# Kernel optimization log

Hardware: AMD Instinct MI355X
Metric: run time of the kernel (lower is better)

Reference implementation:

```python
import jax, jax.numpy as jnp
import numpy as np

V, E, B, K = 100000, 128, 65536, 10


def setup_inputs() -> dict:
    key = jax.random.key(0)
    k1, k2, k3, k4 = jax.random.split(key, 4)
    center_words = jax.random.randint(k1, (B,), 0, V, dtype=jnp.int64 if jax.config.jax_enable_x64 else jnp.int32)
    outside_words = jax.random.randint(k2, (B,), 0, V, dtype=center_words.dtype)
    # torch.multinomial over uniform noise_dist == uniform sampling of negatives
    neg_input_ids = jax.random.randint(k3, (B, K), 0, V, dtype=center_words.dtype)
    # word_embeddings.weight.data.uniform_(-1, 1)
    emb = jax.random.uniform(k4, (V, E), dtype=jnp.float32, minval=-1.0, maxval=1.0)
    return {"center_words": center_words, "outside_words": outside_words,
            "neg_input_ids": neg_input_ids, "emb": emb}


def reference(center_words, outside_words, neg_input_ids, emb):
    em_center = emb[center_words]            # [B, E]
    em_outside = emb[outside_words]          # [B, E]
    pos_dot = jnp.sum(em_center * em_outside, axis=1)          # [B]
    true_pair_loss = -jax.nn.log_sigmoid(pos_dot)              # [B]
    em_neg = emb[neg_input_ids]                                # [B, K, E]
    neg_dot = -jnp.einsum('bke,be->bk', em_neg, em_center)     # [B, K]
    noise_pair_loss = -jnp.sum(jax.nn.log_sigmoid(neg_dot), axis=1)  # [B]
    return jnp.mean(true_pair_loss + noise_pair_loss)
```

## Files before the change

### kernel.cpp

```cpp
#include <hip/hip_runtime.h>
#include <math.h>
#include <stdint.h>

#define BB 65536
#define KK 10
#define EE 128
#define VV 100000

constexpr int BLOCK = 256;
constexpr int BPB   = 32;
constexpr int GRID  = BB / BPB;

constexpr size_t TBL_OFF   = 32768;
constexpr size_t TBL_BYTES = (size_t)VV * EE;

__device__ __forceinline__ float softplus_f(float x) {
    float ax = fabsf(x);
    return fmaxf(x, 0.0f) + __logf(1.0f + __expf(-ax));
}

__global__ __launch_bounds__(256) void
convert_fp8_kernel(const float* __restrict__ emb, uint4* __restrict__ tbl) {
    const int nq = VV * EE / 16;
    const int stride = gridDim.x * blockDim.x;
    for (int q = blockIdx.x * blockDim.x + threadIdx.x; q < nq; q += stride) {
        const float4* src = (const float4*)emb + (size_t)q * 4;
        const float4 f0 = src[0], f1 = src[1], f2 = src[2], f3 = src[3];
        uint32_t w[4];
        {
            int v = 0;
            v = __builtin_amdgcn_cvt_pk_fp8_f32(f0.x, f0.y, v, false);
            v = __builtin_amdgcn_cvt_pk_fp8_f32(f0.z, f0.w, v, true);
            w[0] = (uint32_t)v;
            v = 0;
            v = __builtin_amdgcn_cvt_pk_fp8_f32(f1.x, f1.y, v, false);
            v = __builtin_amdgcn_cvt_pk_fp8_f32(f1.z, f1.w, v, true);
            w[1] = (uint32_t)v;
            v = 0;
            v = __builtin_amdgcn_cvt_pk_fp8_f32(f2.x, f2.y, v, false);
            v = __builtin_amdgcn_cvt_pk_fp8_f32(f2.z, f2.w, v, true);
            w[2] = (uint32_t)v;
            v = 0;
            v = __builtin_amdgcn_cvt_pk_fp8_f32(f3.x, f3.y, v, false);
            v = __builtin_amdgcn_cvt_pk_fp8_f32(f3.z, f3.w, v, true);
            w[3] = (uint32_t)v;
        }
        tbl[q] = make_uint4(w[0], w[1], w[2], w[3]);
    }
}

__device__ __forceinline__ void decode16(const uint4& u, float* f) {
    const uint32_t a[4] = {u.x, u.y, u.z, u.w};
    #pragma unroll
    for (int i = 0; i < 4; ++i) {
        auto lo = __builtin_amdgcn_cvt_pk_f32_fp8((int)a[i], false);
        auto hi = __builtin_amdgcn_cvt_pk_f32_fp8((int)a[i], true);
        f[4 * i + 0] = lo[0];
        f[4 * i + 1] = lo[1];
        f[4 * i + 2] = hi[0];
        f[4 * i + 3] = hi[1];
    }
}

__device__ __forceinline__ float dotd16(const float* cf, const uint4& u) {
    const uint32_t a[4] = {u.x, u.y, u.z, u.w};
    float s = 0.0f;
    #pragma unroll
    for (int i = 0; i < 4; ++i) {
        auto lo = __builtin_amdgcn_cvt_pk_f32_fp8((int)a[i], false);
        auto hi = __builtin_amdgcn_cvt_pk_f32_fp8((int)a[i], true);
        s = fmaf(cf[4 * i + 0], lo[0], s);
        s = fmaf(cf[4 * i + 1], lo[1], s);
        s = fmaf(cf[4 * i + 2], hi[0], s);
        s = fmaf(cf[4 * i + 3], hi[1], s);
    }
    return s;
}

__global__ __launch_bounds__(BLOCK) void
w2v_loss_fp8_kernel(const int* __restrict__ cw,
                    const int* __restrict__ ow,
                    const int* __restrict__ neg,
                    const uint4* __restrict__ rows,
                    float* __restrict__ partial) {
    const int tid = threadIdx.x;
    const int li  = tid & 7;
    const int grp = tid >> 3;
    const int b   = blockIdx.x * BPB + grp;

    const int c = cw[b];
    const int o = ow[b];

    const uint4 ec = rows[(size_t)c * 8 + li];
    float cf[16];
    decode16(ec, cf);

    const uint4 eo = rows[(size_t)o * 8 + li];
    float pd = dotd16(cf, eo);

    float nd[KK];
    #pragma unroll
    for (int k = 0; k < KK; ++k) {
        const int n = neg[b * KK + k];
        const uint4 en = rows[(size_t)n * 8 + li];
        nd[k] = dotd16(cf, en);
    }

    #pragma unroll
    for (int s = 1; s < 8; s <<= 1) {
        pd += __shfl_xor(pd, s);
        #pragma unroll
        for (int k = 0; k < KK; ++k) nd[k] += __shfl_xor(nd[k], s);
    }

    float loss = softplus_f(-pd);
    #pragma unroll
    for (int k = 0; k < KK; ++k) loss += softplus_f(nd[k]);

    __shared__ float smem[BPB];
    if (li == 0) smem[grp] = loss;
    __syncthreads();
    if (tid == 0) {
        float s = 0.0f;
        #pragma unroll
        for (int g = 0; g < BPB; ++g) s += smem[g];
        partial[blockIdx.x] = s;
    }
}

__device__ __forceinline__ float dot8(const float4& a0, const float4& a1,
                                      const float4& b0, const float4& b1) {
    float s = a0.x * b0.x;
    s = fmaf(a0.y, b0.y, s); s = fmaf(a0.z, b0.z, s); s = fmaf(a0.w, b0.w, s);
    s = fmaf(a1.x, b1.x, s); s = fmaf(a1.y, b1.y, s);
    s = fmaf(a1.z, b1.z, s); s = fmaf(a1.w, b1.w, s);
    return s;
}

__global__ __launch_bounds__(BLOCK) void
w2v_loss_f32_kernel(const int* __restrict__ cw,
                    const int* __restrict__ ow,
                    const int* __restrict__ neg,
                    const float* __restrict__ emb,
                    float* __restrict__ partial) {
    const int tid = threadIdx.x;
    const int li  = tid & 15;
    const int grp = tid >> 4;
    const int b   = blockIdx.x * 16 + grp;

    const int c = cw[b];
    const int o = ow[b];
    const float4* ebase = (const float4*)emb;
    const size_t f4 = (size_t)li * 2;

    const float4 ec0 = ebase[(size_t)c * 32 + f4];
    const float4 ec1 = ebase[(size_t)c * 32 + f4 + 1];
    const float4 eo0 = ebase[(size_t)o * 32 + f4];
    const float4 eo1 = ebase[(size_t)o * 32 + f4 + 1];

    float pd = dot8(ec0, ec1, eo0, eo1);
    float nd[KK];
    #pragma unroll
    for (int k = 0; k < KK; ++k) {
        const int n = neg[b * KK + k];
        const float4 en0 = ebase[(size_t)n * 32 + f4];
        const float4 en1 = ebase[(size_t)n * 32 + f4 + 1];
        nd[k] = dot8(ec0, ec1, en0, en1);
    }
    #pragma unroll
    for (int s = 1; s < 16; s <<= 1) {
        pd += __shfl_xor(pd, s);
        #pragma unroll
        for (int k = 0; k < KK; ++k) nd[k] += __shfl_xor(nd[k], s);
    }
    float loss = softplus_f(-pd);
    #pragma unroll
    for (int k = 0; k < KK; ++k) loss += softplus_f(nd[k]);

    __shared__ float smem[16];
    if (li == 0) smem[grp] = loss;
    __syncthreads();
    if (tid == 0) {
        float s = 0.0f;
        #pragma unroll
        for (int g = 0; g < 16; ++g) s += smem[g];
        partial[blockIdx.x] = s;
    }
}

__global__ __launch_bounds__(256) void
w2v_reduce_kernel(const float* __restrict__ partial, int n, float* __restrict__ out) {
    __shared__ float smem[256];
    float s = 0.0f;
    for (int i = threadIdx.x; i < n; i += 256) s += partial[i];
    smem[threadIdx.x] = s;
    __syncthreads();
    for (int step = 128; step > 0; step >>= 1) {
        if (threadIdx.x < step) smem[threadIdx.x] += smem[threadIdx.x + step];
        __syncthreads();
    }
    if (threadIdx.x == 0) out[0] = smem[0] / (float)BB;
}

extern "C" void kernel_launch(void* const* d_in, const int* in_sizes, int n_in,
                              void* d_out, int out_size, void* d_ws, size_t ws_size,
                              hipStream_t stream) {
    const int*   cw  = (const int*)d_in[0];
    const int*   ow  = (const int*)d_in[1];
    const int*   neg = (const int*)d_in[2];
    const float* emb = (const float*)d_in[3];
    float* out     = (float*)d_out;
    float* partial = (float*)d_ws;

    if (ws_size >= TBL_OFF + TBL_BYTES) {
        uint4* tbl = (uint4*)((char*)d_ws + TBL_OFF);
        convert_fp8_kernel<<<2048, 256, 0, stream>>>(emb, tbl);
        w2v_loss_fp8_kernel<<<GRID, BLOCK, 0, stream>>>(cw, ow, neg, tbl, partial);
        w2v_reduce_kernel<<<1, 256, 0, stream>>>(partial, GRID, out);
    } else {
        w2v_loss_f32_kernel<<<BB / 16, BLOCK, 0, stream>>>(cw, ow, neg, emb, partial);
        w2v_reduce_kernel<<<1, 256, 0, stream>>>(partial, BB / 16, out);
    }
}
```

Before: 32.92 us.

## Fold final reduction into loss kernel via atomics and stage indices in LDS

Removes the separate single-block reduce kernel: the convert kernel zeroes the output and each loss block atomically adds its scaled partial sum. Index arrays for each block are loaded cooperatively into shared memory, and all negative rows are gathered before any decoding so the loads can overlap. It also sets a launch-bounds occupancy hint. This trades one kernel launch and a serial tail for 2048 float atomics on one address, which also makes the summation order nondeterministic.

Measured after the change: 49.58 us. 1.51x slower.

```diff
diff --git a/kernel.cpp b/kernel.cpp
--- a/kernel.cpp
+++ b/kernel.cpp
@@ -20,31 +20,32 @@
 }
 
 __global__ __launch_bounds__(256) void
-convert_fp8_kernel(const float* __restrict__ emb, uint4* __restrict__ tbl) {
+convert_fp8_kernel(const float* __restrict__ emb, uint4* __restrict__ tbl,
+                   float* __restrict__ out) {
+    if (blockIdx.x == 0 && threadIdx.x == 0) out[0] = 0.0f;
     const int nq = VV * EE / 16;
     const int stride = gridDim.x * blockDim.x;
     for (int q = blockIdx.x * blockDim.x + threadIdx.x; q < nq; q += stride) {
         const float4* src = (const float4*)emb + (size_t)q * 4;
         const float4 f0 = src[0], f1 = src[1], f2 = src[2], f3 = src[3];
         uint32_t w[4];
-        {
-            int v = 0;
-            v = __builtin_amdgcn_cvt_pk_fp8_f32(f0.x, f0.y, v, false);
-            v = __builtin_amdgcn_cvt_pk_fp8_f32(f0.z, f0.w, v, true);
-            w[0] = (uint32_t)v;
-            v = 0;
-            v = __builtin_amdgcn_cvt_pk_fp8_f32(f1.x, f1.y, v, false);
-            v = __builtin_amdgcn_cvt_pk_fp8_f32(f1.z, f1.w, v, true);
-            w[1] = (uint32_t)v;
-            v = 0;
-            v = __builtin_amdgcn_cvt_pk_fp8_f32(f2.x, f2.y, v, false);
-            v = __builtin_amdgcn_cvt_pk_fp8_f32(f2.z, f2.w, v, true);
-            w[2] = (uint32_t)v;
-            v = 0;
-            v = __builtin_amdgcn_cvt_pk_fp8_f32(f3.x, f3.y, v, false);
-            v = __builtin_amdgcn_cvt_pk_fp8_f32(f3.z, f3.w, v, true);
-            w[3] = (uint32_t)v;
-        }
+        int v;
+        v = 0;
+        v = __builtin_amdgcn_cvt_pk_fp8_f32(f0.x, f0.y, v, false);
+        v = __builtin_amdgcn_cvt_pk_fp8_f32(f0.z, f0.w, v, true);
+        w[0] = (uint32_t)v;
+        v = 0;
+        v = __builtin_amdgcn_cvt_pk_fp8_f32(f1.x, f1.y, v, false);
+        v = __builtin_amdgcn_cvt_pk_fp8_f32(f1.z, f1.w, v, true);
+        w[1] = (uint32_t)v;
+        v = 0;
+        v = __builtin_amdgcn_cvt_pk_fp8_f32(f2.x, f2.y, v, false);
+        v = __builtin_amdgcn_cvt_pk_fp8_f32(f2.z, f2.w, v, true);
+        w[2] = (uint32_t)v;
+        v = 0;
+        v = __builtin_amdgcn_cvt_pk_fp8_f32(f3.x, f3.y, v, false);
+        v = __builtin_amdgcn_cvt_pk_fp8_f32(f3.z, f3.w, v, true);
+        w[3] = (uint32_t)v;
         tbl[q] = make_uint4(w[0], w[1], w[2], w[3]);
     }
 }
@@ -77,34 +78,40 @@
     return s;
 }
 
-__global__ __launch_bounds__(BLOCK) void
+__global__ __launch_bounds__(BLOCK, 4) void
 w2v_loss_fp8_kernel(const int* __restrict__ cw,
                     const int* __restrict__ ow,
                     const int* __restrict__ neg,
                     const uint4* __restrict__ rows,
-                    float* __restrict__ partial) {
+                    float* __restrict__ out) {
     const int tid = threadIdx.x;
     const int li  = tid & 7;
     const int grp = tid >> 3;
-    const int b   = blockIdx.x * BPB + grp;
-
-    const int c = cw[b];
-    const int o = ow[b];
-
+    const int b0  = blockIdx.x * BPB;
+
+    __shared__ int s_cw[BPB];
+    __shared__ int s_ow[BPB];
+    __shared__ int s_neg[BPB * KK];
+    if (tid < BPB)              s_cw[tid]       = cw[b0 + tid];
+    else if (tid < 2 * BPB)     s_ow[tid - BPB] = ow[b0 + tid - BPB];
+    for (int i = tid; i < BPB * KK; i += BLOCK) s_neg[i] = neg[b0 * KK + i];
+    __syncthreads();
+
+    const int c = s_cw[grp];
+    const int o = s_ow[grp];
     const uint4 ec = rows[(size_t)c * 8 + li];
+    const uint4 eo = rows[(size_t)o * 8 + li];
+    uint4 en[KK];
+    #pragma unroll
+    for (int k = 0; k < KK; ++k)
+        en[k] = rows[(size_t)s_neg[grp * KK + k] * 8 + li];
+
     float cf[16];
     decode16(ec, cf);
-
-    const uint4 eo = rows[(size_t)o * 8 + li];
     float pd = dotd16(cf, eo);
-
     float nd[KK];
     #pragma unroll
-    for (int k = 0; k < KK; ++k) {
-        const int n = neg[b * KK + k];
-        const uint4 en = rows[(size_t)n * 8 + li];
-        nd[k] = dotd16(cf, en);
-    }
+    for (int k = 0; k < KK; ++k) nd[k] = dotd16(cf, en[k]);
 
     #pragma unroll
     for (int s = 1; s < 8; s <<= 1) {
@@ -124,7 +131,7 @@
         float s = 0.0f;
         #pragma unroll
         for (int g = 0; g < BPB; ++g) s += smem[g];
-        partial[blockIdx.x] = s;
+        atomicAdd(out, s * (1.0f / (float)BB));
     }
 }
 
@@ -209,15 +216,14 @@
     const int*   ow  = (const int*)d_in[1];
     const int*   neg = (const int*)d_in[2];
     const float* emb = (const float*)d_in[3];
-    float* out     = (float*)d_out;
-    float* partial = (float*)d_ws;
+    float* out = (float*)d_out;
 
     if (ws_size >= TBL_OFF + TBL_BYTES) {
         uint4* tbl = (uint4*)((char*)d_ws + TBL_OFF);
-        convert_fp8_kernel<<<2048, 256, 0, stream>>>(emb, tbl);
-        w2v_loss_fp8_kernel<<<GRID, BLOCK, 0, stream>>>(cw, ow, neg, tbl, partial);
-        w2v_reduce_kernel<<<1, 256, 0, stream>>>(partial, GRID, out);
+        convert_fp8_kernel<<<2048, 256, 0, stream>>>(emb, tbl, out);
+        w2v_loss_fp8_kernel<<<GRID, BLOCK, 0, stream>>>(cw, ow, neg, tbl, out);
     } else {
+        float* partial = (float*)d_ws;
         w2v_loss_f32_kernel<<<BB / 16, BLOCK, 0, stream>>>(cw, ow, neg, emb, partial);
         w2v_reduce_kernel<<<1, 256, 0, stream>>>(partial, BB / 16, out);
     }
```
